# Optimization experiments

Measured on AMD Instinct MI355X. Metric: run time of the kernel, lower is better.

The kernel has to match this reference:

```python
import jax, jax.numpy as jnp
import numpy as np

NUM_HEADS = 24
HEAD_DIM = 128
EPS = 1e-6


def setup_inputs() -> dict:
    key = jax.random.key(0)
    k0, k1, k2 = jax.random.split(key, 3)
    B, S, dim = 2, 2048, 3072
    hidden_states = jax.random.normal(k0, (B, S, dim), dtype=jnp.float32)
    image_rotary_emb = jax.random.normal(k1, (1, 1, S, HEAD_DIM // 2, 2, 2), dtype=jnp.float32)
    w_qkv = jax.random.normal(k2, (dim, 3 * dim), dtype=jnp.float32) * 0.02
    b_qkv = jnp.zeros((3 * dim,), dtype=jnp.float32)
    norm_q_w = jnp.ones((HEAD_DIM,), dtype=jnp.float32)
    norm_k_w = jnp.ones((HEAD_DIM,), dtype=jnp.float32)
    return {
        "hidden_states": hidden_states,
        "image_rotary_emb": image_rotary_emb,
        "w_qkv": w_qkv,
        "b_qkv": b_qkv,
        "norm_q_w": norm_q_w,
        "norm_k_w": norm_k_w,
    }


def _rmsnorm(x, w):
    # RMSNorm over last dim (head_dim)
    var = jnp.mean(x * x, axis=-1, keepdims=True)
    return x * jax.lax.rsqrt(var + EPS) * w


def _apply_rope(x, freqs_cis):
    # x: [B,H,S,D]; freqs_cis: [1,1,S,D//2,2,2]
    B, H, S, D = x.shape
    x_ = x.reshape(B, H, S, D // 2, 1, 2)
    out = freqs_cis[..., 0] * x_[..., 0] + freqs_cis[..., 1] * x_[..., 1]  # [B,H,S,D//2,2]
    return out.reshape(B, H, S, D)


def reference(hidden_states, image_rotary_emb, w_qkv, b_qkv, norm_q_w, norm_k_w):
    B, S, _ = hidden_states.shape
    H, D = NUM_HEADS, HEAD_DIM
    qkv = hidden_states @ w_qkv + b_qkv                 # [B,S,3*H*D]
    qkv = qkv.reshape(B, S, 3, H, D)
    q = jnp.moveaxis(qkv[:, :, 0], 1, 2)                # [B,H,S,D]
    k = jnp.moveaxis(qkv[:, :, 1], 1, 2)
    v = jnp.moveaxis(qkv[:, :, 2], 1, 2)
    q = _rmsnorm(q, norm_q_w)
    k = _rmsnorm(k, norm_k_w)
    q = _apply_rope(q, image_rotary_emb)
    k = _apply_rope(k, image_rotary_emb)
    scale = 1.0 / jnp.sqrt(jnp.asarray(D, dtype=q.dtype))
    scores = jnp.einsum("bhqd,bhkd->bhqk", q, k) * scale
    attn = jax.nn.softmax(scores, axis=-1)
    out = jnp.einsum("bhqk,bhkd->bhqd", attn, v)        # [B,H,S,D]
    out = jnp.moveaxis(out, 1, 2).reshape(B, S, H * D)  # [B,S,H*D]
    return out
```

## Files before the change

kernel.cpp:

```cpp
#include <hip/hip_runtime.h>


#define SS 2048
#define BB 2
#define HH 24
#define DD 128
#define KDIM 3072
#define N3 9216
#define MM 4096
#define NT 96

typedef float f32x4 __attribute__((ext_vector_type(4)));
typedef __bf16 bf16x8 __attribute__((ext_vector_type(8)));

__device__ __forceinline__ unsigned short f2b(float f) {
  union { float f; unsigned int u; } v; v.f = f;
  unsigned int u = v.u;
  u += 0x7FFFu + ((u >> 16) & 1u);
  return (unsigned short)(u >> 16);
}
__device__ __forceinline__ float b2f(unsigned short b) {
  union { unsigned int u; float f; } v; v.u = ((unsigned int)b) << 16; return v.f;
}
__device__ __forceinline__ f32x4 mfma16(bf16x8 a, bf16x8 b, f32x4 c) {
  return __builtin_amdgcn_mfma_f32_16x16x32_bf16(a, b, c, 0, 0, 0);
}
typedef __attribute__((address_space(1))) void gas_void;
typedef __attribute__((address_space(3))) void las_void;
__device__ __forceinline__ void load_lds16(const void* g, void* l) {
  __builtin_amdgcn_global_load_lds((gas_void*)g, (las_void*)l, 16, 0, 0);
}
__device__ __forceinline__ int swz(int row, int byteInRow) {
  return byteInRow ^ ((row & 7) << 4);
}

__global__ void cvt_bf16(const float* __restrict__ in, unsigned short* __restrict__ out, int n4) {
  int i = blockIdx.x * 256 + threadIdx.x;
  if (i >= n4) return;
  float4 v = reinterpret_cast<const float4*>(in)[i];
  ushort4 o;
  o.x = f2b(v.x); o.y = f2b(v.y); o.z = f2b(v.z); o.w = f2b(v.w);
  reinterpret_cast<ushort4*>(out)[i] = o;
}

__global__ void transpose_w(const float* __restrict__ w, unsigned short* __restrict__ wt) {
  __shared__ float tile[32][33];
  int n0 = blockIdx.x * 32, k0 = blockIdx.y * 32;
  int tx = threadIdx.x, ty = threadIdx.y;
#pragma unroll
  for (int i = 0; i < 4; i++)
    tile[ty + 8 * i][tx] = w[(size_t)(k0 + ty + 8 * i) * N3 + n0 + tx];
  __syncthreads();
#pragma unroll
  for (int i = 0; i < 4; i++)
    wt[(size_t)(n0 + ty + 8 * i) * KDIM + k0 + tx] = f2b(tile[tx][ty + 8 * i]);
}

__global__ __launch_bounds__(512, 2) void gemm_qkv(
    const unsigned short* __restrict__ A, const unsigned short* __restrict__ Bt,
    const float* __restrict__ bias, unsigned short* __restrict__ qkv) {
  __shared__ __align__(16) unsigned short As[2][8192];
  __shared__ __align__(16) unsigned short Bs[2][8192];
  const int tid = threadIdx.x;
  const int wave = tid >> 6, lane = tid & 63;
  const int wm = wave >> 2, wn = wave & 3;
  const int g = lane >> 4, lr = lane & 15;
  const int swzid = (blockIdx.x & 7) * 72 + (blockIdx.x >> 3);
  const int m0 = (swzid & 15) * 256, n0 = (swzid >> 4) * 256;
  const unsigned short* Ag = A + (size_t)m0 * KDIM;
  const unsigned short* Bg = Bt + (size_t)n0 * KDIM;

  f32x4 acc[8][4] = {};
  const int srow = lane >> 2;
  const int sks = (lane & 3) * 8;

#pragma unroll
  for (int cc = 0; cc < 2; cc++) {
    int c = wave * 2 + cc;
    int m = c * 16 + srow;
    load_lds16(Ag + (size_t)m * KDIM + sks, &As[0][c * 512]);
    load_lds16(Bg + (size_t)m * KDIM + sks, &Bs[0][c * 512]);
  }

#define GTILE(K0, CUR, DOST, NK0, NXT, VM)                                     \
  {                                                                            \
    __builtin_amdgcn_s_barrier();                                              \
    __builtin_amdgcn_sched_barrier(0);                                         \
    if (DOST) {                                                                \
      _Pragma("unroll") for (int cc = 0; cc < 2; cc++) {                       \
        int c = wave * 2 + cc;                                                 \
        int m = c * 16 + srow;                                                 \
        load_lds16(Ag + (size_t)m * KDIM + (NK0) + sks, &As[NXT][c * 512]);    \
        load_lds16(Bg + (size_t)m * KDIM + (NK0) + sks, &Bs[NXT][c * 512]);    \
      }                                                                        \
    }                                                                          \
    asm volatile("s_waitcnt vmcnt(" #VM ")" ::: "memory");                     \
    __builtin_amdgcn_sched_barrier(0);                                         \
    bf16x8 af[8], bfr[4];                                                      \
    _Pragma("unroll") for (int i = 0; i < 8; i++)                              \
      af[i] = *reinterpret_cast<const bf16x8*>(                                \
          &As[CUR][(wm * 128 + i * 16 + lr) * 32 + g * 8]);                    \
    _Pragma("unroll") for (int j = 0; j < 4; j++)                              \
      bfr[j] = *reinterpret_cast<const bf16x8*>(                               \
          &Bs[CUR][(wn * 64 + j * 16 + lr) * 32 + g * 8]);                     \
    __builtin_amdgcn_s_setprio(1);                                             \
    _Pragma("unroll") for (int i = 0; i < 8; i++)                              \
      _Pragma("unroll") for (int j = 0; j < 4; j++)                            \
        acc[i][j] = mfma16(af[i], bfr[j], acc[i][j]);                          \
    __builtin_amdgcn_s_setprio(0);                                             \
  }

  for (int t = 0; t < NT - 4; t += 2) {
    GTILE(t * 32, 0, 1, (t + 1) * 32, 1, 4);
    GTILE((t + 1) * 32, 1, 1, (t + 2) * 32, 0, 4);
  }
  GTILE((NT - 4) * 32, 0, 1, (NT - 3) * 32, 1, 4);
  GTILE((NT - 3) * 32, 1, 1, (NT - 2) * 32, 0, 4);
  GTILE((NT - 2) * 32, 0, 1, (NT - 1) * 32, 1, 4);
  GTILE((NT - 1) * 32, 1, 0, 0, 0, 0);
#undef GTILE

#pragma unroll
  for (int j = 0; j < 4; j++) {
    int ng = n0 + wn * 64 + j * 16 + lr;
    int which = ng / 3072;
    int rem = ng - which * 3072;
    int h = rem >> 7, d = rem & 127;
    float bv = bias[ng];
#pragma unroll
    for (int i = 0; i < 8; i++) {
#pragma unroll
      for (int r = 0; r < 4; r++) {
        int m = m0 + wm * 128 + i * 16 + g * 4 + r;
        int b = m >> 11, s = m & 2047;
        qkv[((((size_t)which * BB + b) * HH + h) * SS + s) * DD + d] =
            f2b(acc[i][j][r] + bv);
      }
    }
  }
}

__global__ void rms_rope(unsigned short* qkv, const float* __restrict__ freqs,
                         const float* __restrict__ wq, const float* __restrict__ wk) {
  int row = blockIdx.x * 4 + (threadIdx.x >> 6);
  int lane = threadIdx.x & 63;
  int s = row & 2047;
  int t = row >> 11;
  int which = t / (BB * HH);
  unsigned short* x = qkv + (size_t)row * DD;
  ushort2 xx = *reinterpret_cast<ushort2*>(&x[lane * 2]);
  float x0 = b2f(xx.x), x1 = b2f(xx.y);
  float ssum = x0 * x0 + x1 * x1;
#pragma unroll
  for (int off = 1; off < 64; off <<= 1) ssum += __shfl_xor(ssum, off);
  float rn = rsqrtf(ssum * (1.0f / 128.0f) + 1e-6f);
  const float* wgt = which ? wk : wq;
  x0 *= rn * wgt[lane * 2];
  x1 *= rn * wgt[lane * 2 + 1];
  float4 f = reinterpret_cast<const float4*>(freqs)[s * 64 + lane];
  ushort2 yy;
  yy.x = f2b(f.x * x0 + f.y * x1);
  yy.y = f2b(f.z * x0 + f.w * x1);
  *reinterpret_cast<ushort2*>(&x[lane * 2]) = yy;
}

__global__ void transpose_v(const unsigned short* __restrict__ qkv, unsigned short* __restrict__ vt) {
  __shared__ unsigned short tile[32][33];
  int bh = blockIdx.z;
  int s0 = blockIdx.x * 32, d0 = blockIdx.y * 32;
  const unsigned short* v = qkv + ((size_t)2 * BB * HH + bh) * SS * DD;
  int tx = threadIdx.x, ty = threadIdx.y;
#pragma unroll
  for (int i = 0; i < 4; i++)
    tile[ty + 8 * i][tx] = v[(size_t)(s0 + ty + 8 * i) * DD + d0 + tx];
  __syncthreads();
  unsigned short* o = vt + (size_t)bh * DD * SS;
#pragma unroll
  for (int i = 0; i < 4; i++)
    o[(size_t)(d0 + ty + 8 * i) * SS + s0 + tx] = tile[tx][ty + 8 * i];
}

__global__ __launch_bounds__(256, 2) void attn(
    const unsigned short* __restrict__ qkv, const unsigned short* __restrict__ vt,
    float* __restrict__ out) {
  __shared__ __align__(16) unsigned short Ks[64 * 128];
  __shared__ __align__(16) unsigned short Vs[128 * 64];
  __shared__ __align__(16) unsigned short Ps[4][16 * 64];
  const int bh = blockIdx.y;
  const int q0 = blockIdx.x * 64;
  const int wave = threadIdx.x >> 6, lane = threadIdx.x & 63;
  const int g = lane >> 4, lr = lane & 15;
  const unsigned short* Q   = qkv + (size_t)bh * SS * DD;
  const unsigned short* Kp  = qkv + ((size_t)BB * HH + bh) * SS * DD;
  const unsigned short* Vtp = vt + (size_t)bh * DD * SS;

  bf16x8 qf[4];
  {
    int qr = q0 + wave * 16 + lr;
#pragma unroll
    for (int kd = 0; kd < 4; kd++)
      qf[kd] = *reinterpret_cast<const bf16x8*>(&Q[(size_t)qr * DD + kd * 32 + g * 8]);
  }
  float mrow[4], lrow[4];
  f32x4 o[8] = {};
#pragma unroll
  for (int r = 0; r < 4; r++) { mrow[r] = -1e30f; lrow[r] = 0.f; }
  const float scale = 0.08838834764831845f;

  for (int kt = 0; kt < SS / 64; kt++) {
    int k0 = kt * 64;
    __syncthreads();
#pragma unroll
    for (int i = 0; i < 4; i++) {
      int c = wave * 4 + i;
      {
        int row = c * 4 + g;
        int lb = swz(row, lr * 16);
        load_lds16(Kp + (size_t)(k0 + row) * DD + (lb >> 1), &Ks[c * 512]);
      }
      {
        int row = c * 8 + (lane >> 3);
        int lb = swz(row, (lane & 7) * 16);
        load_lds16(Vtp + (size_t)row * SS + k0 + (lb >> 1), &Vs[c * 512]);
      }
    }
    __syncthreads();

    f32x4 sc[4] = {};
#pragma unroll
    for (int cf = 0; cf < 4; cf++) {
#pragma unroll
      for (int kd = 0; kd < 4; kd++) {
        int row = cf * 16 + lr;
        bf16x8 kb = *reinterpret_cast<const bf16x8*>(
            &Ks[(row * 256 + swz(row, kd * 64 + g * 16)) >> 1]);
        sc[cf] = mfma16(qf[kd], kb, sc[cf]);
      }
    }
#pragma unroll
    for (int cf = 0; cf < 4; cf++) sc[cf] *= scale;

#pragma unroll
    for (int r = 0; r < 4; r++) {
      float pm = fmaxf(fmaxf(sc[0][r], sc[1][r]), fmaxf(sc[2][r], sc[3][r]));
      pm = fmaxf(pm, __shfl_xor(pm, 1));
      pm = fmaxf(pm, __shfl_xor(pm, 2));
      pm = fmaxf(pm, __shfl_xor(pm, 4));
      pm = fmaxf(pm, __shfl_xor(pm, 8));
      float mnew = fmaxf(mrow[r], pm);
      float corr = __expf(mrow[r] - mnew);
      float psum = 0.f;
      int prow = g * 4 + r;
#pragma unroll
      for (int cf = 0; cf < 4; cf++) {
        float p = __expf(sc[cf][r] - mnew);
        psum += p;
        int col = cf * 16 + lr;
        Ps[wave][(prow * 128 + swz(prow, col * 2)) >> 1] = f2b(p);
      }
      psum += __shfl_xor(psum, 1);
      psum += __shfl_xor(psum, 2);
      psum += __shfl_xor(psum, 4);
      psum += __shfl_xor(psum, 8);
      lrow[r] = lrow[r] * corr + psum;
      mrow[r] = mnew;
#pragma unroll
      for (int dn = 0; dn < 8; dn++) o[dn][r] *= corr;
    }

#pragma unroll
    for (int ks = 0; ks < 2; ks++) {
      bf16x8 pa = *reinterpret_cast<const bf16x8*>(
          &Ps[wave][(lr * 128 + swz(lr, ks * 64 + g * 16)) >> 1]);
#pragma unroll
      for (int dn = 0; dn < 8; dn++) {
        int vrow = dn * 16 + lr;
        bf16x8 vb = *reinterpret_cast<const bf16x8*>(
            &Vs[(vrow * 128 + swz(vrow, ks * 64 + g * 16)) >> 1]);
        o[dn] = mfma16(pa, vb, o[dn]);
      }
    }
  }

  const int b = bh / HH, h = bh % HH;
#pragma unroll
  for (int r = 0; r < 4; r++) {
    int s = q0 + wave * 16 + g * 4 + r;
    float inv = 1.0f / lrow[r];
#pragma unroll
    for (int dn = 0; dn < 8; dn++) {
      int d = dn * 16 + lr;
      out[((size_t)b * SS + s) * 3072 + h * DD + d] = o[dn][r] * inv;
    }
  }
}

extern "C" void kernel_launch(void* const* d_in, const int* in_sizes, int n_in,
                              void* d_out, int out_size, void* d_ws, size_t ws_size,
                              hipStream_t stream) {
  const float* hs     = (const float*)d_in[0];
  const float* freqs  = (const float*)d_in[1];
  const float* w_qkv  = (const float*)d_in[2];
  const float* b_qkv  = (const float*)d_in[3];
  const float* norm_q = (const float*)d_in[4];
  const float* norm_k = (const float*)d_in[5];
  float* out = (float*)d_out;

  char* ws = (char*)d_ws;
  unsigned short* A_bf = (unsigned short*)(ws);
  unsigned short* Wt   = (unsigned short*)(ws + 25165824);
  unsigned short* qkv  = (unsigned short*)(ws + 81788928);
  unsigned short* Vt   = (unsigned short*)(ws + 157286400);

  cvt_bf16<<<dim3(12288), dim3(256), 0, stream>>>(hs, A_bf, 3145728);
  transpose_w<<<dim3(288, 96), dim3(32, 8), 0, stream>>>(w_qkv, Wt);
  gemm_qkv<<<dim3(576), dim3(512), 0, stream>>>(A_bf, Wt, b_qkv, qkv);
  rms_rope<<<dim3(49152), dim3(256), 0, stream>>>(qkv, freqs, norm_q, norm_k);
  transpose_v<<<dim3(64, 4, 48), dim3(32, 8), 0, stream>>>(qkv, Vt);
  attn<<<dim3(32, 48), dim3(256), 0, stream>>>(qkv, Vt, out);
}
```

Before: 839.4 us.

## Restructure QKV GEMM mainloop with K=64 tiles, swizzled LDS, interleaved staging

The QKV projection GEMM main loop now uses K-tiles of 64 instead of 32, doubling LDS buffers to 64KB per operand pair. Global-to-LDS loads for A and B are split into half-tiles and interleaved between quarter-sized MFMA blocks, with XOR swizzling of LDS columns to avoid bank conflicts. The aim is to hide load latency and reduce barrier overhead per unit of math. In exchange it adds many more barriers per tile and raises LDS usage, which may limit occupancy to the requested 2 blocks per CU.

```diff
diff --git a/kernel.cpp b/kernel.cpp
--- a/kernel.cpp
+++ b/kernel.cpp
@@ -8,7 +8,6 @@
 #define KDIM 3072
 #define N3 9216
 #define MM 4096
-#define NT 96
 
 typedef float f32x4 __attribute__((ext_vector_type(4)));
 typedef __bf16 bf16x8 __attribute__((ext_vector_type(8)));
@@ -59,8 +58,8 @@
 __global__ __launch_bounds__(512, 2) void gemm_qkv(
     const unsigned short* __restrict__ A, const unsigned short* __restrict__ Bt,
     const float* __restrict__ bias, unsigned short* __restrict__ qkv) {
-  __shared__ __align__(16) unsigned short As[2][8192];
-  __shared__ __align__(16) unsigned short Bs[2][8192];
+  __shared__ __align__(16) unsigned short As[2][16384];
+  __shared__ __align__(16) unsigned short Bs[2][16384];
   const int tid = threadIdx.x;
   const int wave = tid >> 6, lane = tid & 63;
   const int wm = wave >> 2, wn = wave & 3;
@@ -71,54 +70,104 @@
   const unsigned short* Bg = Bt + (size_t)n0 * KDIM;
 
   f32x4 acc[8][4] = {};
-  const int srow = lane >> 2;
-  const int sks = (lane & 3) * 8;
-
-#pragma unroll
-  for (int cc = 0; cc < 2; cc++) {
-    int c = wave * 2 + cc;
-    int m = c * 16 + srow;
-    load_lds16(Ag + (size_t)m * KDIM + sks, &As[0][c * 512]);
-    load_lds16(Bg + (size_t)m * KDIM + sks, &Bs[0][c * 512]);
-  }
-
-#define GTILE(K0, CUR, DOST, NK0, NXT, VM)                                     \
-  {                                                                            \
-    __builtin_amdgcn_s_barrier();                                              \
-    __builtin_amdgcn_sched_barrier(0);                                         \
-    if (DOST) {                                                                \
-      _Pragma("unroll") for (int cc = 0; cc < 2; cc++) {                       \
-        int c = wave * 2 + cc;                                                 \
-        int m = c * 16 + srow;                                                 \
-        load_lds16(Ag + (size_t)m * KDIM + (NK0) + sks, &As[NXT][c * 512]);    \
-        load_lds16(Bg + (size_t)m * KDIM + (NK0) + sks, &Bs[NXT][c * 512]);    \
-      }                                                                        \
-    }                                                                          \
-    asm volatile("s_waitcnt vmcnt(" #VM ")" ::: "memory");                     \
-    __builtin_amdgcn_sched_barrier(0);                                         \
-    bf16x8 af[8], bfr[4];                                                      \
-    _Pragma("unroll") for (int i = 0; i < 8; i++)                              \
-      af[i] = *reinterpret_cast<const bf16x8*>(                                \
-          &As[CUR][(wm * 128 + i * 16 + lr) * 32 + g * 8]);                    \
-    _Pragma("unroll") for (int j = 0; j < 4; j++)                              \
-      bfr[j] = *reinterpret_cast<const bf16x8*>(                               \
-          &Bs[CUR][(wn * 64 + j * 16 + lr) * 32 + g * 8]);                     \
+  const int srow = lane >> 3;
+  const int scolU = ((lane & 7) * 8) ^ ((lane & 32) ? 16 : 0);
+
+#define STAGE(arr, buf, half, src, kt)                                         \
+  do {                                                                         \
+    load_lds16((src) + (size_t)((half)*128 + wave * 8 + srow) * KDIM +         \
+                   (kt)*64 + scolU,                                            \
+               &arr[buf][(half)*8192 + wave * 512]);                           \
+    load_lds16((src) + (size_t)((half)*128 + (8 + wave) * 8 + srow) * KDIM +   \
+                   (kt)*64 + scolU,                                            \
+               &arr[buf][(half)*8192 + (8 + wave) * 512]);                     \
+  } while (0)
+
+#define LDA(b, r, c) (*reinterpret_cast<const bf16x8*>(                        \
+    &As[b][(r)*64 + (((c) ^ ((((r) >> 2) & 1) << 4)))]))
+#define LDB(b, r, c) (*reinterpret_cast<const bf16x8*>(                        \
+    &Bs[b][(r)*64 + (((c) ^ ((((r) >> 2) & 1) << 4)))]))
+
+  bf16x8 af[4][2], bfr[4][2];
+#define READA(b, RO)                                                           \
+  _Pragma("unroll") for (int i2 = 0; i2 < 4; i2++)                             \
+  _Pragma("unroll") for (int k2 = 0; k2 < 2; k2++)                             \
+      af[i2][k2] = LDA(b, wm * 128 + ((RO) + i2) * 16 + lr, k2 * 32 + g * 8);
+#define READB(b, CO)                                                           \
+  _Pragma("unroll") for (int j2 = 0; j2 < 2; j2++)                             \
+  _Pragma("unroll") for (int k2 = 0; k2 < 2; k2++)                             \
+      bfr[(CO) + j2][k2] = LDB(b, wn * 64 + ((CO) + j2) * 16 + lr, k2 * 32 + g * 8);
+#define MFMAQ(RO, CO)                                                          \
+  do {                                                                         \
     __builtin_amdgcn_s_setprio(1);                                             \
-    _Pragma("unroll") for (int i = 0; i < 8; i++)                              \
-      _Pragma("unroll") for (int j = 0; j < 4; j++)                            \
-        acc[i][j] = mfma16(af[i], bfr[j], acc[i][j]);                          \
+    _Pragma("unroll") for (int i2 = 0; i2 < 4; i2++)                           \
+    _Pragma("unroll") for (int j2 = 0; j2 < 2; j2++)                           \
+    _Pragma("unroll") for (int k2 = 0; k2 < 2; k2++)                           \
+        acc[(RO) + i2][(CO) + j2] =                                            \
+            mfma16(af[i2][k2], bfr[(CO) + j2][k2], acc[(RO) + i2][(CO) + j2]); \
     __builtin_amdgcn_s_setprio(0);                                             \
-  }
-
-  for (int t = 0; t < NT - 4; t += 2) {
-    GTILE(t * 32, 0, 1, (t + 1) * 32, 1, 4);
-    GTILE((t + 1) * 32, 1, 1, (t + 2) * 32, 0, 4);
-  }
-  GTILE((NT - 4) * 32, 0, 1, (NT - 3) * 32, 1, 4);
-  GTILE((NT - 3) * 32, 1, 1, (NT - 2) * 32, 0, 4);
-  GTILE((NT - 2) * 32, 0, 1, (NT - 1) * 32, 1, 4);
-  GTILE((NT - 1) * 32, 1, 0, 0, 0, 0);
-#undef GTILE
+  } while (0)
+#define BARR __builtin_amdgcn_s_barrier()
+#define LGKM0 asm volatile("s_waitcnt lgkmcnt(0)" ::: "memory")
+#define VMC(n) asm volatile("s_waitcnt vmcnt(" #n ")" ::: "memory")
+
+  STAGE(As, 0, 0, Ag, 0);  STAGE(As, 0, 1, Ag, 0);
+  STAGE(Bs, 0, 0, Bg, 0);  STAGE(Bs, 0, 1, Bg, 0);
+  STAGE(Bs, 1, 0, Bg, 1);  STAGE(Bs, 1, 1, Bg, 1);
+  VMC(4);
+  BARR;
+
+  for (int t = 0; t < 46; t += 2) {
+    READA(0, 0); READB(0, 0);
+    STAGE(As, 1, 0, Ag, t + 1);
+    BARR; LGKM0; MFMAQ(0, 0); BARR;
+    READB(0, 2);
+    STAGE(As, 1, 1, Ag, t + 1);
+    BARR; LGKM0; MFMAQ(0, 2); BARR;
+    READA(0, 4);
+    STAGE(Bs, 0, 0, Bg, t + 2);
+    BARR; LGKM0; MFMAQ(4, 0); BARR;
+    STAGE(Bs, 0, 1, Bg, t + 2);
+    BARR; MFMAQ(4, 2); VMC(4); BARR;
+    READA(1, 0); READB(1, 0);
+    STAGE(As, 0, 0, Ag, t + 2);
+    BARR; LGKM0; MFMAQ(0, 0); BARR;
+    READB(1, 2);
+    STAGE(As, 0, 1, Ag, t + 2);
+    BARR; LGKM0; MFMAQ(0, 2); BARR;
+    READA(1, 4);
+    STAGE(Bs, 1, 0, Bg, t + 3);
+    BARR; LGKM0; MFMAQ(4, 0); BARR;
+    STAGE(Bs, 1, 1, Bg, t + 3);
+    BARR; MFMAQ(4, 2); VMC(4); BARR;
+  }
+  {
+    READA(0, 0); READB(0, 0);
+    STAGE(As, 1, 0, Ag, 47);
+    BARR; LGKM0; MFMAQ(0, 0); BARR;
+    READB(0, 2);
+    STAGE(As, 1, 1, Ag, 47);
+    BARR; LGKM0; MFMAQ(0, 2); BARR;
+    READA(0, 4);
+    BARR; LGKM0; MFMAQ(4, 0); BARR;
+    BARR; MFMAQ(4, 2); VMC(0); BARR;
+    READA(1, 0); READB(1, 0);
+    BARR; LGKM0; MFMAQ(0, 0); BARR;
+    READB(1, 2);
+    BARR; LGKM0; MFMAQ(0, 2); BARR;
+    READA(1, 4);
+    BARR; LGKM0; MFMAQ(4, 0); BARR;
+    MFMAQ(4, 2);
+  }
+#undef STAGE
+#undef LDA
+#undef LDB
+#undef READA
+#undef READB
+#undef MFMAQ
+#undef BARR
+#undef LGKM0
+#undef VMC
 
 #pragma unroll
   for (int j = 0; j < 4; j++) {
```

After: 798.5 us. 1.05x faster.
